# Kernel tuning notes

Measured on AMD Instinct MI355X. Metric: run time of the kernel, lower is better.

Reference implementation:

```python
import jax, jax.numpy as jnp
import numpy as np

N, E = 50000, 800000
IN, HID, OUT, H = 128, 32, 32, 4
NEG_SLOPE = 0.2
EPS = 1e-5


def layernorm(x, g, b):
    mu = x.mean(-1, keepdims=True)
    var = ((x - mu) ** 2).mean(-1, keepdims=True)
    return (x - mu) * jax.lax.rsqrt(var + EPS) * g + b


def gat_conv(x, src, dst, W, a_s, a_d, bias, heads, ch, concat):
    n = x.shape[0]
    h = (x @ W).reshape(n, heads, ch)               # [N,H,C]
    alpha_s = (h * a_s).sum(-1)                     # [N,H]
    alpha_d = (h * a_d).sum(-1)                     # [N,H]
    e = jax.nn.leaky_relu(alpha_s[src] + alpha_d[dst], NEG_SLOPE)  # [E,H]
    m = jax.ops.segment_max(e, dst, num_segments=n)
    m = jnp.where(jnp.isfinite(m), m, 0.0)
    ex = jnp.exp(e - m[dst])
    denom = jax.ops.segment_sum(ex, dst, num_segments=n)
    alpha = ex / (denom[dst] + 1e-16)               # [E,H]
    msg = h[src] * alpha[:, :, None]                # [E,H,C]
    out = jax.ops.segment_sum(msg, dst, num_segments=n)  # [N,H,C]
    out = out.reshape(n, heads * ch) if concat else out.mean(axis=1)
    return out + bias


def setup_inputs() -> dict:
    key = jax.random.key(0)
    ks = jax.random.split(key, 24)
    HC = HID * H
    s = 0.05
    inp = {
        "x": jax.random.normal(ks[0], (N, IN), jnp.float32),
        "edge_index": jax.random.randint(ks[1], (2, E), 0, N),
        "W1": jax.random.normal(ks[2], (IN, HC), jnp.float32) * s,
        "as1": jax.random.normal(ks[3], (H, HID), jnp.float32) * s,
        "ad1": jax.random.normal(ks[4], (H, HID), jnp.float32) * s,
        "b1": jnp.zeros((HC,), jnp.float32),
        "g1": jnp.ones((HC,), jnp.float32),
        "be1": jnp.zeros((HC,), jnp.float32),
        "W2": jax.random.normal(ks[5], (HC, HC), jnp.float32) * s,
        "as2": jax.random.normal(ks[6], (H, HID), jnp.float32) * s,
        "ad2": jax.random.normal(ks[7], (H, HID), jnp.float32) * s,
        "b2": jnp.zeros((HC,), jnp.float32),
        "g2": jnp.ones((HC,), jnp.float32),
        "be2": jnp.zeros((HC,), jnp.float32),
        "W3": jax.random.normal(ks[8], (HC, OUT * H), jnp.float32) * s,
        "as3": jax.random.normal(ks[9], (H, OUT), jnp.float32) * s,
        "ad3": jax.random.normal(ks[10], (H, OUT), jnp.float32) * s,
        "b3": jnp.zeros((OUT,), jnp.float32),
        "Wsk": jax.random.normal(ks[11], (IN, HC), jnp.float32) * s,
        "bsk": jnp.zeros((HC,), jnp.float32),
    }
    return inp


def reference(x, edge_index, W1, as1, ad1, b1, g1, be1, W2, as2, ad2, b2, g2, be2, W3, as3, ad3, b3, Wsk, bsk):
    n = x.shape[0]
    loops = jnp.arange(n, dtype=edge_index.dtype)
    src = jnp.concatenate([edge_index[0], loops])
    dst = jnp.concatenate([edge_index[1], loops])
    h = gat_conv(x, src, dst, W1, as1, ad1, b1, H, HID, True)
    h = jax.nn.elu(h)
    h = layernorm(h, g1, be1)
    h = h + (x @ Wsk + bsk)  # residual (dropout is identity in eval)
    h = gat_conv(h, src, dst, W2, as2, ad2, b2, H, HID, True)
    h = jax.nn.elu(h)
    h = layernorm(h, g2, be2)
    h = gat_conv(h, src, dst, W3, as3, ad3, b3, H, OUT, False)
    return h
```

## Files before the change

kernel.cpp:

```cpp
#include <hip/hip_runtime.h>
#include <hip/hip_bf16.h>

typedef __attribute__((ext_vector_type(8))) short short8;
typedef __attribute__((ext_vector_type(4))) float f32x4;
using bf16 = __hip_bfloat16;

#define NEG_SLOPE 0.2f
#define LN_EPS 1e-5f

__device__ __forceinline__ unsigned short f2bfu(float v) {
    bf16 t = __float2bfloat16(v);
    unsigned short s;
    __builtin_memcpy(&s, &t, 2);
    return s;
}
__device__ __forceinline__ short f2bf(float v) {
    bf16 t = __float2bfloat16(v);
    short s;
    __builtin_memcpy(&s, &t, 2);
    return s;
}
__device__ __forceinline__ unsigned packbf(float a, float b) {
    return (unsigned)f2bfu(a) | ((unsigned)f2bfu(b) << 16);
}
__device__ __forceinline__ float bflo(unsigned u) { return __uint_as_float(u << 16); }
__device__ __forceinline__ float bfhi(unsigned u) { return __uint_as_float(u & 0xffff0000u); }
__device__ __forceinline__ float bf1(unsigned short u) { return __uint_as_float(((unsigned)u) << 16); }

__global__ void detect_k(const void* __restrict__ x, int* flag,
                         int* bucketCur, int CAP) {
    int lane = threadIdx.x;
    for (int i = lane; i < 512; i += 64) bucketCur[i] = i * CAP;
    const unsigned short* u = (const unsigned short*)x;
    float m = 0.f;
    for (int i = lane; i < 8192; i += 64) {
        float v = fabsf(bf1(u[i]));
        if (!(v == v)) v = 1e30f;
        m = fmaxf(m, v);
    }
    for (int d = 1; d < 64; d <<= 1) m = fmaxf(m, __shfl_xor(m, d));
    if (lane == 0) flag[0] = (m > 1e4f) ? 1 : 0;
}

struct Ptr4 { const void* p[4]; };
struct Ptr14 { const void* p[14]; };
struct Ptr3 { const void* p[3]; };
struct Ptr6 { const void* p[6]; };
__global__ void stage_k(Ptr4 Ws, bf16* __restrict__ WT,
                        Ptr14 ptrs, bf16* __restrict__ sv,
                        Ptr3 Wv, Ptr6 av, bf16* __restrict__ vaT,
                        const int* __restrict__ flag) {
    int b = blockIdx.x;
    int f = flag[0];
    if (b < 256) {
        int gid = b * 256 + threadIdx.x;
        int m = gid >> 14;
        int idx = gid & 16383;
        int i = idx >> 7, j = idx & 127;
        const void* W = Ws.p[m];
        float v = f ? ((const float*)W)[idx]
                    : __bfloat162float(((const bf16*)W)[idx]);
        WT[m * 16384 + j * 128 + i] = __float2bfloat16(v);
    } else if (b == 256) {
        for (int k = threadIdx.x; k < 14 * 128; k += 256) {
            int t = k >> 7, i = k & 127;
            int n = (t == 12) ? 32 : 128;
            if (i < n) {
                const void* s = ptrs.p[t];
                float v = f ? ((const float*)s)[i]
                            : __bfloat162float(((const bf16*)s)[i]);
                sv[k] = __float2bfloat16(v);
            }
        }
    } else {
        int gid = (b - 257) * 256 + threadIdx.x;
        int l = gid >> 11;
        if (l >= 3) return;
        int c = (gid >> 7) & 15, k = gid & 127;
        float acc = 0.f;
        if (c < 8) {
            int hd = c & 3;
            const void* W = Wv.p[l];
            const void* a = av.p[l * 2 + (c >> 2)];
            for (int j = 0; j < 32; ++j) {
                float wv = f ? ((const float*)W)[k * 128 + hd * 32 + j]
                             : __bfloat162float(((const bf16*)W)[k * 128 + hd * 32 + j]);
                float avv = f ? ((const float*)a)[hd * 32 + j]
                              : __bfloat162float(((const bf16*)a)[hd * 32 + j]);
                acc += wv * avv;
            }
        }
        vaT[gid] = __float2bfloat16(acc);
    }
}

#define SCAT_EPB 2048
__global__ __launch_bounds__(256) void bscatter_k(const int* __restrict__ src,
                                                  const int* __restrict__ dst,
                                                  int* bucketCur,
                                                  int* __restrict__ ebuf,
                                                  int E, int NB, int CAP) {
    __shared__ int lcnt[512], lbase[512];
    int t = threadIdx.x;
    int e0 = blockIdx.x * SCAT_EPB;
    int cnt = E - e0;
    if (cnt > SCAT_EPB) cnt = SCAT_EPB;
    for (int i = t; i < NB; i += 256) lcnt[i] = 0;
    __syncthreads();
    for (int i = t; i < cnt; i += 256)
        atomicAdd(&lcnt[dst[e0 + i] >> 7], 1);
    __syncthreads();
    for (int i = t; i < NB; i += 256) {
        int c = lcnt[i];
        lbase[i] = c ? atomicAdd(&bucketCur[i], c) : 0;
        lcnt[i] = 0;
    }
    __syncthreads();
    for (int i = t; i < cnt; i += 256) {
        int d = dst[e0 + i];
        int b = d >> 7;
        int pos = lbase[b] + atomicAdd(&lcnt[b], 1);
        if (pos < (b + 1) * CAP)
            ebuf[pos] = ((d & 127) << 16) | src[e0 + i];
    }
}

__global__ __launch_bounds__(256) void build_k(const int* __restrict__ ebuf,
                                               const int* __restrict__ bucketCur,
                                               int* __restrict__ rowSE,
                                               int* __restrict__ colSrc,
                                               int N, int CAP) {
    int b = blockIdx.x, t = threadIdx.x;
    int base = b * CAP;
    int cnt = bucketCur[b] - base;
    if (cnt > CAP) cnt = CAP;
    __shared__ int nodeCnt[128], nodeCur[128], ws2[2];
    if (t < 128) nodeCnt[t] = 0;
    __syncthreads();
    for (int i = t; i < cnt; i += 256)
        atomicAdd(&nodeCnt[ebuf[base + i] >> 16], 1);
    __syncthreads();
    int v = 0, incl = 0;
    if (t < 128) {
        v = nodeCnt[t];
        incl = v;
        for (int d = 1; d < 64; d <<= 1) {
            int u = __shfl_up(incl, d);
            if ((t & 63) >= d) incl += u;
        }
        if ((t & 63) == 63) ws2[t >> 6] = incl;
    }
    __syncthreads();
    if (t < 128) {
        int excl = incl - v + ((t >= 64) ? ws2[0] : 0);
        int node = b * 128 + t;
        if (node < N) {
            rowSE[node * 2] = base + excl;
            rowSE[node * 2 + 1] = base + excl + v;
        }
        nodeCur[t] = excl;
    }
    __syncthreads();
    for (int i = t; i < cnt; i += 256) {
        int p = ebuf[base + i];
        int pos = base + atomicAdd(&nodeCur[p >> 16], 1);
        colSrc[pos] = (p & 0xffff) << 8;
    }
    for (int i = cnt + t; i < CAP; i += 256)
        colSrc[base + i] = 0;
}

template <int DUAL>
__global__ __launch_bounds__(256) void gemm_k(const void* __restrict__ A,
                                              const bf16* __restrict__ WT,
                                              bf16* __restrict__ out0,
                                              bf16* __restrict__ out1,
                                              const bf16* __restrict__ bias1,
                                              const bf16* __restrict__ vaT,
                                              float* __restrict__ asN,
                                              float* __restrict__ adN,
                                              int N, const int* __restrict__ flag) {
    int wave = threadIdx.x >> 6, lane = threadIdx.x & 63;
    int lm = lane & 15, lk = lane >> 4;
    const short* Ws = (const short*)WT;
    const short* Vs = (const short*)vaT;
    bool f32m = flag && flag[0];

    short8 bw0[2][4], bw1[DUAL ? 2 : 1][DUAL ? 4 : 1];
#pragma unroll
    for (int ct = 0; ct < 2; ++ct) {
        int c = (wave * 2 + ct) * 16 + lm;
#pragma unroll
        for (int kk = 0; kk < 4; ++kk)
            bw0[ct][kk] = *(const short8*)(Ws + (size_t)c * 128 + kk * 32 + lk * 8);
    }
    if (DUAL) {
#pragma unroll
        for (int ct = 0; ct < 2; ++ct) {
            int c = (wave * 2 + ct) * 16 + lm;
#pragma unroll
            for (int kk = 0; kk < 4; ++kk)
                bw1[ct][kk] = *(const short8*)(Ws + 16384 + (size_t)c * 128 + kk * 32 + lk * 8);
        }
    }
    short8 va8[4];
    if (wave == 0) {
#pragma unroll
        for (int kk = 0; kk < 4; ++kk)
            va8[kk] = *(const short8*)(Vs + (size_t)lm * 128 + kk * 32 + lk * 8);
    }
    float bv[DUAL ? 2 : 1];
    if (DUAL) {
#pragma unroll
        for (int ct = 0; ct < 2; ++ct)
            bv[ct] = __bfloat162float(bias1[(wave * 2 + ct) * 16 + lm]);
    }

    int stride = gridDim.x * 32;
    for (int rowBase = blockIdx.x * 32; rowBase < N; rowBase += stride) {
        short8 af[2][4];
#pragma unroll
        for (int rt = 0; rt < 2; ++rt) {
            int r = rowBase + rt * 16 + lm;
            if (r >= N) r = N - 1;
            if (f32m) {
#pragma unroll
                for (int kk = 0; kk < 4; ++kk) {
                    const float* Af = (const float*)A + (size_t)r * 128 + kk * 32 + lk * 8;
                    float4 q0 = *(const float4*)(Af);
                    float4 q1 = *(const float4*)(Af + 4);
                    short8 v;
                    v[0] = f2bf(q0.x); v[1] = f2bf(q0.y); v[2] = f2bf(q0.z); v[3] = f2bf(q0.w);
                    v[4] = f2bf(q1.x); v[5] = f2bf(q1.y); v[6] = f2bf(q1.z); v[7] = f2bf(q1.w);
                    af[rt][kk] = v;
                }
            } else {
#pragma unroll
                for (int kk = 0; kk < 4; ++kk)
                    af[rt][kk] = *(const short8*)((const short*)A + (size_t)r * 128 + kk * 32 + lk * 8);
            }
        }

        f32x4 acc0[2][2];
        f32x4 acc1[DUAL ? 2 : 1][DUAL ? 2 : 1];
#pragma unroll
        for (int ct = 0; ct < 2; ++ct)
#pragma unroll
            for (int rt = 0; rt < 2; ++rt) acc0[ct][rt] = (f32x4){0.f, 0.f, 0.f, 0.f};
        if (DUAL) {
#pragma unroll
            for (int ct = 0; ct < 2; ++ct)
#pragma unroll
                for (int rt = 0; rt < 2; ++rt) acc1[ct][rt] = (f32x4){0.f, 0.f, 0.f, 0.f};
        }

#pragma unroll
        for (int rt = 0; rt < 2; ++rt) {
#pragma unroll
            for (int kk = 0; kk < 4; ++kk) {
                acc0[0][rt] = __builtin_amdgcn_mfma_f32_16x16x32_bf16(af[rt][kk], bw0[0][kk], acc0[0][rt], 0, 0, 0);
                acc0[1][rt] = __builtin_amdgcn_mfma_f32_16x16x32_bf16(af[rt][kk], bw0[1][kk], acc0[1][rt], 0, 0, 0);
                if (DUAL) {
                    acc1[0][rt] = __builtin_amdgcn_mfma_f32_16x16x32_bf16(af[rt][kk], bw1[0][kk], acc1[0][rt], 0, 0, 0);
                    acc1[1][rt] = __builtin_amdgcn_mfma_f32_16x16x32_bf16(af[rt][kk], bw1[1][kk], acc1[1][rt], 0, 0, 0);
                }
            }
        }

#pragma unroll
        for (int ct = 0; ct < 2; ++ct) {
            int c = (wave * 2 + ct) * 16 + lm;
#pragma unroll
            for (int rt = 0; rt < 2; ++rt) {
#pragma unroll
                for (int i = 0; i < 4; ++i) {
                    int r = rowBase + rt * 16 + lk * 4 + i;
                    if (r < N) out0[(size_t)r * 128 + c] = __float2bfloat16(acc0[ct][rt][i]);
                }
            }
        }
        if (DUAL) {
#pragma unroll
            for (int ct = 0; ct < 2; ++ct) {
                int c = (wave * 2 + ct) * 16 + lm;
#pragma unroll
                for (int rt = 0; rt < 2; ++rt) {
#pragma unroll
                    for (int i = 0; i < 4; ++i) {
                        int r = rowBase + rt * 16 + lk * 4 + i;
                        if (r < N) out1[(size_t)r * 128 + c] = __float2bfloat16(acc1[ct][rt][i] + bv[ct]);
                    }
                }
            }
        }

        if (wave == 0) {
            f32x4 accA[2];
#pragma unroll
            for (int rt = 0; rt < 2; ++rt) accA[rt] = (f32x4){0.f, 0.f, 0.f, 0.f};
#pragma unroll
            for (int rt = 0; rt < 2; ++rt)
#pragma unroll
                for (int kk = 0; kk < 4; ++kk)
                    accA[rt] = __builtin_amdgcn_mfma_f32_16x16x32_bf16(af[rt][kk], va8[kk], accA[rt], 0, 0, 0);
            if (lm < 8) {
                float* dst = (lm < 4) ? asN : adN;
                int hh = lm & 3;
#pragma unroll
                for (int rt = 0; rt < 2; ++rt)
#pragma unroll
                    for (int i = 0; i < 4; ++i) {
                        int r = rowBase + rt * 16 + lk * 4 + i;
                        if (r < N) dst[(size_t)r * 4 + hh] = accA[rt][i];
                    }
            }
        }
    }
}

template <int MODE>
__global__ __launch_bounds__(256) void agg_k(const bf16* __restrict__ h,
                                             const float* __restrict__ asN,
                                             const float* __restrict__ adN,
                                             const int* __restrict__ rowSE,
                                             const int* __restrict__ colSrc,
                                             const bf16* __restrict__ bvec,
                                             const bf16* __restrict__ g,
                                             const bf16* __restrict__ be,
                                             void* outv, int N,
                                             const int* __restrict__ flag) {
    int wv = threadIdx.x >> 6, lane = threadIdx.x & 63;
    int n = blockIdx.x * 4 + wv;
    if (n >= N) return;
    int grp = lane >> 4, t = lane & 15;
    int hd = t >> 2;
    const char* hbase = (const char*)h + t * 16;
    const char* abase = (const char*)asN + hd * 4;

    int2 se = ((const int2*)rowSE)[n];
    int st = se.x, en = se.y;
    if (en < st) en = st;

    uint4 hself = *(const uint4*)(hbase + (size_t)n * 256);
    float adn = adN[(size_t)n * 4 + hd];
    float asn_self = asN[(size_t)n * 4 + hd];

    float a[8];
#pragma unroll
    for (int k = 0; k < 8; ++k) a[k] = 0.f;
    float den = 0.f;

    int j = st + grp;
    int off = (j < en) ? colSrc[j] : 0;
    float av = *(const float*)(abase + (off >> 4));
    uint4 hq = *(const uint4*)(hbase + off);
    for (; j < en; j += 4) {
        int off2 = colSrc[j + 4];
        float av2 = *(const float*)(abase + (off2 >> 4));
        uint4 hq2 = *(const uint4*)(hbase + off2);
        float e = av + adn;
        float w = __expf(fmaxf(e, NEG_SLOPE * e));
        den += w;
        a[0] += w * bflo(hq.x); a[1] += w * bfhi(hq.x);
        a[2] += w * bflo(hq.y); a[3] += w * bfhi(hq.y);
        a[4] += w * bflo(hq.z); a[5] += w * bfhi(hq.z);
        a[6] += w * bflo(hq.w); a[7] += w * bfhi(hq.w);
        av = av2; hq = hq2;
    }

#pragma unroll
    for (int k = 0; k < 8; ++k) {
        a[k] += __shfl_xor(a[k], 16);
        a[k] += __shfl_xor(a[k], 32);
    }
    den += __shfl_xor(den, 16);
    den += __shfl_xor(den, 32);

    float es = asn_self + adn;
    float wsf = __expf(fmaxf(es, NEG_SLOPE * es));
    den += wsf;
    a[0] += wsf * bflo(hself.x); a[1] += wsf * bfhi(hself.x);
    a[2] += wsf * bflo(hself.y); a[3] += wsf * bfhi(hself.y);
    a[4] += wsf * bflo(hself.z); a[5] += wsf * bfhi(hself.z);
    a[6] += wsf * bflo(hself.w); a[7] += wsf * bfhi(hself.w);

    float inv = 1.f / (den + 1e-16f);
    float y[8];
#pragma unroll
    for (int k = 0; k < 8; ++k) y[k] = a[k] * inv;

    if (MODE == 3) {
#pragma unroll
        for (int k = 0; k < 8; ++k) {
            y[k] += __shfl_xor(y[k], 4);
            y[k] += __shfl_xor(y[k], 8);
            y[k] *= 0.25f;
        }
        if (lane < 4) {
            int u = lane;
            uint4 bp = *(const uint4*)((const unsigned short*)bvec + u * 8);
            float v0 = y[0] + bflo(bp.x), v1 = y[1] + bfhi(bp.x);
            float v2 = y[2] + bflo(bp.y), v3 = y[3] + bfhi(bp.y);
            float v4 = y[4] + bflo(bp.z), v5 = y[5] + bfhi(bp.z);
            float v6 = y[6] + bflo(bp.w), v7 = y[7] + bfhi(bp.w);
            if (flag[0]) {
                float4* op = (float4*)outv + (size_t)n * 8 + u * 2;
                op[0] = make_float4(v0, v1, v2, v3);
                op[1] = make_float4(v4, v5, v6, v7);
            } else {
                uint4 pk;
                pk.x = packbf(v0, v1); pk.y = packbf(v2, v3);
                pk.z = packbf(v4, v5); pk.w = packbf(v6, v7);
                ((uint4*)outv)[(size_t)n * 4 + u] = pk;
            }
        }
    } else {
        unsigned short* out = (unsigned short*)outv;
        uint4 bp = *(const uint4*)((const unsigned short*)bvec + t * 8);
        y[0] += bflo(bp.x); y[1] += bfhi(bp.x);
        y[2] += bflo(bp.y); y[3] += bfhi(bp.y);
        y[4] += bflo(bp.z); y[5] += bfhi(bp.z);
        y[6] += bflo(bp.w); y[7] += bfhi(bp.w);
#pragma unroll
        for (int k = 0; k < 8; ++k) y[k] = y[k] > 0.f ? y[k] : (__expf(y[k]) - 1.f);
        float s = 0.f, q = 0.f;
#pragma unroll
        for (int k = 0; k < 8; ++k) { s += y[k]; q += y[k] * y[k]; }
        for (int d = 1; d < 16; d <<= 1) {
            s += __shfl_xor(s, d);
            q += __shfl_xor(q, d);
        }
        float mu = s * (1.f / 128.f);
        float var = q * (1.f / 128.f) - mu * mu;
        var = fmaxf(var, 0.f);
        float rs = rsqrtf(var + LN_EPS);
        if (lane < 16) {
            uint4 gp = *(const uint4*)((const unsigned short*)g + t * 8);
            uint4 ep = *(const uint4*)((const unsigned short*)be + t * 8);
            float z[8];
            z[0] = (y[0] - mu) * rs * bflo(gp.x) + bflo(ep.x);
            z[1] = (y[1] - mu) * rs * bfhi(gp.x) + bfhi(ep.x);
            z[2] = (y[2] - mu) * rs * bflo(gp.y) + bflo(ep.y);
            z[3] = (y[3] - mu) * rs * bfhi(gp.y) + bfhi(ep.y);
            z[4] = (y[4] - mu) * rs * bflo(gp.z) + bflo(ep.z);
            z[5] = (y[5] - mu) * rs * bfhi(gp.z) + bfhi(ep.z);
            z[6] = (y[6] - mu) * rs * bflo(gp.w) + bflo(ep.w);
            z[7] = (y[7] - mu) * rs * bfhi(gp.w) + bfhi(ep.w);
            if (MODE == 1) {
                uint4 sk = *(uint4*)(out + (size_t)n * 128 + t * 8);
                z[0] += bflo(sk.x); z[1] += bfhi(sk.x);
                z[2] += bflo(sk.y); z[3] += bfhi(sk.y);
                z[4] += bflo(sk.z); z[5] += bfhi(sk.z);
                z[6] += bflo(sk.w); z[7] += bfhi(sk.w);
            }
            uint4 pk;
            pk.x = packbf(z[0], z[1]); pk.y = packbf(z[2], z[3]);
            pk.z = packbf(z[4], z[5]); pk.w = packbf(z[6], z[7]);
            *(uint4*)(out + (size_t)n * 128 + t * 8) = pk;
        }
    }
}

extern "C" void kernel_launch(void* const* d_in, const int* in_sizes, int n_in,
                              void* d_out, int out_size, void* d_ws, size_t ws_size,
                              hipStream_t stream) {
    const void* x  = d_in[0];
    const int*  ei = (const int*)d_in[1];

    int N = in_sizes[0] / 128;
    int E = in_sizes[1] / 2;
    const int* srcI = ei;
    const int* dstI = ei + E;

    int NB = (N + 127) >> 7;
    int CAP = (E / NB + 1024 + 511) & ~511;

    char* w = (char*)d_ws;
    size_t o = 0;
    auto carve = [&](size_t bytes) {
        void* p = w + o;
        o += (bytes + 255) & ~(size_t)255;
        return p;
    };
    int*  dtFlag = (int*)carve(256);
    bf16* WTall = (bf16*)carve(4 * 16384 * 2);
    bf16* sv   = (bf16*)carve(14 * 128 * 2);
    bf16* vaT  = (bf16*)carve(3 * 16 * 128 * 2);
    bf16* hB   = (bf16*)carve((size_t)N * 128 * 2);
    bf16* xB   = (bf16*)carve((size_t)N * 128 * 2);
    float* asN = (float*)carve((size_t)N * 4 * 4);
    float* adN = (float*)carve((size_t)N * 4 * 4);
    int* rowSE = (int*)carve((size_t)N * 2 * 4);
    int* colSrc= (int*)carve((size_t)NB * CAP * 4 + 64);
    int* ebuf  = (int*)carve((size_t)NB * CAP * 4);
    int* bucketCur = (int*)carve(512 * 4);

    detect_k<<<1, 64, 0, stream>>>(x, dtFlag, bucketCur, CAP);

    Ptr4 wp;
    wp.p[0] = d_in[2];  wp.p[1] = d_in[18];
    wp.p[2] = d_in[8];  wp.p[3] = d_in[14];
    Ptr14 ptrs;
    ptrs.p[0] = d_in[3];  ptrs.p[1] = d_in[4];  ptrs.p[2] = d_in[5];
    ptrs.p[3] = d_in[6];  ptrs.p[4] = d_in[7];
    ptrs.p[5] = d_in[9];  ptrs.p[6] = d_in[10]; ptrs.p[7] = d_in[11];
    ptrs.p[8] = d_in[12]; ptrs.p[9] = d_in[13];
    ptrs.p[10] = d_in[15]; ptrs.p[11] = d_in[16]; ptrs.p[12] = d_in[17];
    ptrs.p[13] = d_in[19];
    Ptr3 wv3;
    wv3.p[0] = d_in[2]; wv3.p[1] = d_in[8]; wv3.p[2] = d_in[14];
    Ptr6 av6;
    av6.p[0] = d_in[3];  av6.p[1] = d_in[4];
    av6.p[2] = d_in[9];  av6.p[3] = d_in[10];
    av6.p[4] = d_in[15]; av6.p[5] = d_in[16];

    stage_k<<<281, 256, 0, stream>>>(wp, WTall, ptrs, sv, wv3, av6, vaT, dtFlag);

    bscatter_k<<<(E + SCAT_EPB - 1) / SCAT_EPB, 256, 0, stream>>>(srcI, dstI,
                                                                 bucketCur, ebuf, E, NB, CAP);
    build_k<<<NB, 256, 0, stream>>>(ebuf, bucketCur, rowSE, colSrc, N, CAP);

    int gb = (N + 63) / 64;
    int nb4 = (N + 3) / 4;

    gemm_k<1><<<gb, 256, 0, stream>>>(x, WTall, hB, xB, sv + 13 * 128,
                                      vaT, asN, adN, N, dtFlag);
    agg_k<1><<<nb4, 256, 0, stream>>>(hB, asN, adN, rowSE, colSrc,
                                      sv + 2 * 128, sv + 3 * 128, sv + 4 * 128,
                                      xB, N, dtFlag);

    gemm_k<0><<<gb, 256, 0, stream>>>(xB, WTall + 2 * 16384, hB, nullptr, nullptr,
                                      vaT + 2048, asN, adN, N, nullptr);
    agg_k<2><<<nb4, 256, 0, stream>>>(hB, asN, adN, rowSE, colSrc,
                                      sv + 7 * 128, sv + 8 * 128, sv + 9 * 128,
                                      xB, N, dtFlag);

    gemm_k<0><<<gb, 256, 0, stream>>>(xB, WTall + 3 * 16384, hB, nullptr, nullptr,
                                      vaT + 4096, asN, adN, N, nullptr);
    agg_k<3><<<nb4, 256, 0, stream>>>(hB, asN, adN, rowSE, colSrc,
                                      sv + 12 * 128, nullptr, nullptr,
                                      d_out, N, dtFlag);
}
```

Baseline: 350.1 us.

## Vectorize GEMM stores via swapped MFMA operands and deepen aggregation prefetch

Swaps the MFMA A/B operands so each lane holds four consecutive columns of one row, which allows packed 8-byte bf16 stores and 16-byte float4 stores for the attention logits in place of scattered scalar stores. The aggregation loop now prefetches two neighbor edges ahead instead of one, and colSrc gets extra zero padding so the lookahead reads stay in bounds. The epilogue is reworked so every lane finalizes two channels, reducing across the whole wave instead of having 16 lanes each handle eight. The deeper prefetch costs more registers, and the epilogue adds select logic and a longer shuffle chain.

```diff
diff --git a/kernel.cpp b/kernel.cpp
--- a/kernel.cpp
+++ b/kernel.cpp
@@ -166,7 +166,8 @@
         int pos = base + atomicAdd(&nodeCur[p >> 16], 1);
         colSrc[pos] = (p & 0xffff) << 8;
     }
-    for (int i = cnt + t; i < CAP; i += 256)
+    int capz = CAP + ((b == (int)gridDim.x - 1) ? 32 : 0);
+    for (int i = cnt + t; i < capz; i += 256)
         colSrc[base + i] = 0;
 }
 
@@ -209,11 +210,15 @@
         for (int kk = 0; kk < 4; ++kk)
             va8[kk] = *(const short8*)(Vs + (size_t)lm * 128 + kk * 32 + lk * 8);
     }
-    float bv[DUAL ? 2 : 1];
+    float bv[2][4];
     if (DUAL) {
 #pragma unroll
-        for (int ct = 0; ct < 2; ++ct)
-            bv[ct] = __bfloat162float(bias1[(wave * 2 + ct) * 16 + lm]);
+        for (int ct = 0; ct < 2; ++ct) {
+            int c0 = (wave * 2 + ct) * 16 + lk * 4;
+#pragma unroll
+            for (int i = 0; i < 4; ++i)
+                bv[ct][i] = __bfloat162float(bias1[c0 + i]);
+        }
     }
 
     int stride = gridDim.x * 32;
@@ -258,37 +263,41 @@
         for (int rt = 0; rt < 2; ++rt) {
 #pragma unroll
             for (int kk = 0; kk < 4; ++kk) {
-                acc0[0][rt] = __builtin_amdgcn_mfma_f32_16x16x32_bf16(af[rt][kk], bw0[0][kk], acc0[0][rt], 0, 0, 0);
-                acc0[1][rt] = __builtin_amdgcn_mfma_f32_16x16x32_bf16(af[rt][kk], bw0[1][kk], acc0[1][rt], 0, 0, 0);
+                acc0[0][rt] = __builtin_amdgcn_mfma_f32_16x16x32_bf16(bw0[0][kk], af[rt][kk], acc0[0][rt], 0, 0, 0);
+                acc0[1][rt] = __builtin_amdgcn_mfma_f32_16x16x32_bf16(bw0[1][kk], af[rt][kk], acc0[1][rt], 0, 0, 0);
                 if (DUAL) {
-                    acc1[0][rt] = __builtin_amdgcn_mfma_f32_16x16x32_bf16(af[rt][kk], bw1[0][kk], acc1[0][rt], 0, 0, 0);
-                    acc1[1][rt] = __builtin_amdgcn_mfma_f32_16x16x32_bf16(af[rt][kk], bw1[1][kk], acc1[1][rt], 0, 0, 0);
+                    acc1[0][rt] = __builtin_amdgcn_mfma_f32_16x16x32_bf16(bw1[0][kk], af[rt][kk], acc1[0][rt], 0, 0, 0);
+                    acc1[1][rt] = __builtin_amdgcn_mfma_f32_16x16x32_bf16(bw1[1][kk], af[rt][kk], acc1[1][rt], 0, 0, 0);
                 }
             }
         }
 
 #pragma unroll
         for (int ct = 0; ct < 2; ++ct) {
-            int c = (wave * 2 + ct) * 16 + lm;
+            int c0 = (wave * 2 + ct) * 16 + lk * 4;
 #pragma unroll
             for (int rt = 0; rt < 2; ++rt) {
-#pragma unroll
-                for (int i = 0; i < 4; ++i) {
-                    int r = rowBase + rt * 16 + lk * 4 + i;
-                    if (r < N) out0[(size_t)r * 128 + c] = __float2bfloat16(acc0[ct][rt][i]);
+                int r = rowBase + rt * 16 + lm;
+                if (r < N) {
+                    uint2 pk;
+                    pk.x = packbf(acc0[ct][rt][0], acc0[ct][rt][1]);
+                    pk.y = packbf(acc0[ct][rt][2], acc0[ct][rt][3]);
+                    *(uint2*)((unsigned short*)out0 + (size_t)r * 128 + c0) = pk;
                 }
             }
         }
         if (DUAL) {
 #pragma unroll
             for (int ct = 0; ct < 2; ++ct) {
-                int c = (wave * 2 + ct) * 16 + lm;
+                int c0 = (wave * 2 + ct) * 16 + lk * 4;
 #pragma unroll
                 for (int rt = 0; rt < 2; ++rt) {
-#pragma unroll
-                    for (int i = 0; i < 4; ++i) {
-                        int r = rowBase + rt * 16 + lk * 4 + i;
-                        if (r < N) out1[(size_t)r * 128 + c] = __float2bfloat16(acc1[ct][rt][i] + bv[ct]);
+                    int r = rowBase + rt * 16 + lm;
+                    if (r < N) {
+                        uint2 pk;
+                        pk.x = packbf(acc1[ct][rt][0] + bv[ct][0], acc1[ct][rt][1] + bv[ct][1]);
+                        pk.y = packbf(acc1[ct][rt][2] + bv[ct][2], acc1[ct][rt][3] + bv[ct][3]);
+                        *(uint2*)((unsigned short*)out1 + (size_t)r * 128 + c0) = pk;
                     }
                 }
             }
@@ -302,17 +311,14 @@
             for (int rt = 0; rt < 2; ++rt)
 #pragma unroll
                 for (int kk = 0; kk < 4; ++kk)
-                    accA[rt] = __builtin_amdgcn_mfma_f32_16x16x32_bf16(af[rt][kk], va8[kk], accA[rt], 0, 0, 0);
-            if (lm < 8) {
-                float* dst = (lm < 4) ? asN : adN;
-                int hh = lm & 3;
-#pragma unroll
-                for (int rt = 0; rt < 2; ++rt)
-#pragma unroll
-                    for (int i = 0; i < 4; ++i) {
-                        int r = rowBase + rt * 16 + lk * 4 + i;
-                        if (r < N) dst[(size_t)r * 4 + hh] = accA[rt][i];
-                    }
+                    accA[rt] = __builtin_amdgcn_mfma_f32_16x16x32_bf16(va8[kk], af[rt][kk], accA[rt], 0, 0, 0);
+            if (lk < 2) {
+                float* dp = lk ? adN : asN;
+#pragma unroll
+                for (int rt = 0; rt < 2; ++rt) {
+                    int r = rowBase + rt * 16 + lm;
+                    if (r < N) *(f32x4*)(dp + (size_t)r * 4) = accA[rt];
+                }
             }
         }
     }
@@ -341,9 +347,9 @@
     int st = se.x, en = se.y;
     if (en < st) en = st;
 
-    uint4 hself = *(const uint4*)(hbase + (size_t)n * 256);
     float adn = adN[(size_t)n * 4 + hd];
     float asn_self = asN[(size_t)n * 4 + hd];
+    unsigned hs = *(const unsigned*)((const char*)h + (size_t)n * 256 + t * 16 + grp * 4);
 
     float a[8];
 #pragma unroll
@@ -351,21 +357,27 @@
     float den = 0.f;
 
     int j = st + grp;
-    int off = (j < en) ? colSrc[j] : 0;
-    float av = *(const float*)(abase + (off >> 4));
-    uint4 hq = *(const uint4*)(hbase + off);
+    int o0 = (j < en) ? colSrc[j] : 0;
+    int o1 = colSrc[j + 4];
+    int o2 = colSrc[j + 8];
+    float av0 = *(const float*)(abase + (o0 >> 4));
+    uint4 hq0 = *(const uint4*)(hbase + o0);
+    float av1 = *(const float*)(abase + (o1 >> 4));
+    uint4 hq1 = *(const uint4*)(hbase + o1);
     for (; j < en; j += 4) {
-        int off2 = colSrc[j + 4];
-        float av2 = *(const float*)(abase + (off2 >> 4));
-        uint4 hq2 = *(const uint4*)(hbase + off2);
-        float e = av + adn;
+        int o3 = colSrc[j + 12];
+        float av2 = *(const float*)(abase + (o2 >> 4));
+        uint4 hq2 = *(const uint4*)(hbase + o2);
+        float e = av0 + adn;
         float w = __expf(fmaxf(e, NEG_SLOPE * e));
         den += w;
-        a[0] += w * bflo(hq.x); a[1] += w * bfhi(hq.x);
-        a[2] += w * bflo(hq.y); a[3] += w * bfhi(hq.y);
-        a[4] += w * bflo(hq.z); a[5] += w * bfhi(hq.z);
-        a[6] += w * bflo(hq.w); a[7] += w * bfhi(hq.w);
-        av = av2; hq = hq2;
+        a[0] += w * bflo(hq0.x); a[1] += w * bfhi(hq0.x);
+        a[2] += w * bflo(hq0.y); a[3] += w * bfhi(hq0.y);
+        a[4] += w * bflo(hq0.z); a[5] += w * bfhi(hq0.z);
+        a[6] += w * bflo(hq0.w); a[7] += w * bfhi(hq0.w);
+        o2 = o3;
+        av0 = av1; hq0 = hq1;
+        av1 = av2; hq1 = hq2;
     }
 
 #pragma unroll
@@ -379,54 +391,43 @@
     float es = asn_self + adn;
     float wsf = __expf(fmaxf(es, NEG_SLOPE * es));
     den += wsf;
-    a[0] += wsf * bflo(hself.x); a[1] += wsf * bfhi(hself.x);
-    a[2] += wsf * bflo(hself.y); a[3] += wsf * bfhi(hself.y);
-    a[4] += wsf * bflo(hself.z); a[5] += wsf * bfhi(hself.z);
-    a[6] += wsf * bflo(hself.w); a[7] += wsf * bfhi(hself.w);
+
+    float s0 = (grp & 1) ? a[2] : a[0];
+    float s1 = (grp & 1) ? a[3] : a[1];
+    float s2 = (grp & 1) ? a[6] : a[4];
+    float s3 = (grp & 1) ? a[7] : a[5];
+    float p0 = (grp & 2) ? s2 : s0;
+    float p1 = (grp & 2) ? s3 : s1;
+
+    p0 += wsf * bflo(hs);
+    p1 += wsf * bfhi(hs);
 
     float inv = 1.f / (den + 1e-16f);
-    float y[8];
-#pragma unroll
-    for (int k = 0; k < 8; ++k) y[k] = a[k] * inv;
+    float y0 = p0 * inv, y1 = p1 * inv;
 
     if (MODE == 3) {
-#pragma unroll
-        for (int k = 0; k < 8; ++k) {
-            y[k] += __shfl_xor(y[k], 4);
-            y[k] += __shfl_xor(y[k], 8);
-            y[k] *= 0.25f;
-        }
-        if (lane < 4) {
-            int u = lane;
-            uint4 bp = *(const uint4*)((const unsigned short*)bvec + u * 8);
-            float v0 = y[0] + bflo(bp.x), v1 = y[1] + bfhi(bp.x);
-            float v2 = y[2] + bflo(bp.y), v3 = y[3] + bfhi(bp.y);
-            float v4 = y[4] + bflo(bp.z), v5 = y[5] + bfhi(bp.z);
-            float v6 = y[6] + bflo(bp.w), v7 = y[7] + bfhi(bp.w);
+        y0 += __shfl_xor(y0, 4); y0 += __shfl_xor(y0, 8); y0 *= 0.25f;
+        y1 += __shfl_xor(y1, 4); y1 += __shfl_xor(y1, 8); y1 *= 0.25f;
+        if (t < 4) {
+            int oc = t * 8 + grp * 2;
+            unsigned bp = *(const unsigned*)((const char*)bvec + oc * 2);
+            float v0 = y0 + bflo(bp), v1 = y1 + bfhi(bp);
             if (flag[0]) {
-                float4* op = (float4*)outv + (size_t)n * 8 + u * 2;
-                op[0] = make_float4(v0, v1, v2, v3);
-                op[1] = make_float4(v4, v5, v6, v7);
+                *(float2*)((float*)outv + (size_t)n * 32 + oc) = make_float2(v0, v1);
             } else {
-                uint4 pk;
-                pk.x = packbf(v0, v1); pk.y = packbf(v2, v3);
-                pk.z = packbf(v4, v5); pk.w = packbf(v6, v7);
-                ((uint4*)outv)[(size_t)n * 4 + u] = pk;
+                ((unsigned*)outv)[(size_t)n * 16 + (oc >> 1)] = packbf(v0, v1);
             }
         }
     } else {
         unsigned short* out = (unsigned short*)outv;
-        uint4 bp = *(const uint4*)((const unsigned short*)bvec + t * 8);
-        y[0] += bflo(bp.x); y[1] += bfhi(bp.x);
-        y[2] += bflo(bp.y); y[3] += bfhi(bp.y);
-        y[4] += bflo(bp.z); y[5] += bfhi(bp.z);
-        y[6] += bflo(bp.w); y[7] += bfhi(bp.w);
-#pragma unroll
-        for (int k = 0; k < 8; ++k) y[k] = y[k] > 0.f ? y[k] : (__expf(y[k]) - 1.f);
-        float s = 0.f, q = 0.f;
-#pragma unroll
-        for (int k = 0; k < 8; ++k) { s += y[k]; q += y[k] * y[k]; }
-        for (int d = 1; d < 16; d <<= 1) {
+        int boff = t * 16 + grp * 4;
+        unsigned bp = *(const unsigned*)((const char*)bvec + boff);
+        y0 += bflo(bp); y1 += bfhi(bp);
+        y0 = y0 > 0.f ? y0 : (__expf(y0) - 1.f);
+        y1 = y1 > 0.f ? y1 : (__expf(y1) - 1.f);
+        float s = y0 + y1, q = y0 * y0 + y1 * y1;
+#pragma unroll
+        for (int d = 1; d < 64; d <<= 1) {
             s += __shfl_xor(s, d);
             q += __shfl_xor(q, d);
         }
@@ -434,30 +435,16 @@
         float var = q * (1.f / 128.f) - mu * mu;
         var = fmaxf(var, 0.f);
         float rs = rsqrtf(var + LN_EPS);
-        if (lane < 16) {
-            uint4 gp = *(const uint4*)((const unsigned short*)g + t * 8);
-            uint4 ep = *(const uint4*)((const unsigned short*)be + t * 8);
-            float z[8];
-            z[0] = (y[0] - mu) * rs * bflo(gp.x) + bflo(ep.x);
-            z[1] = (y[1] - mu) * rs * bfhi(gp.x) + bfhi(ep.x);
-            z[2] = (y[2] - mu) * rs * bflo(gp.y) + bflo(ep.y);
-            z[3] = (y[3] - mu) * rs * bfhi(gp.y) + bfhi(ep.y);
-            z[4] = (y[4] - mu) * rs * bflo(gp.z) + bflo(ep.z);
-            z[5] = (y[5] - mu) * rs * bfhi(gp.z) + bfhi(ep.z);
-            z[6] = (y[6] - mu) * rs * bflo(gp.w) + bflo(ep.w);
-            z[7] = (y[7] - mu) * rs * bfhi(gp.w) + bfhi(ep.w);
-            if (MODE == 1) {
-                uint4 sk = *(uint4*)(out + (size_t)n * 128 + t * 8);
-                z[0] += bflo(sk.x); z[1] += bfhi(sk.x);
-                z[2] += bflo(sk.y); z[3] += bfhi(sk.y);
-                z[4] += bflo(sk.z); z[5] += bfhi(sk.z);
-                z[6] += bflo(sk.w); z[7] += bfhi(sk.w);
-            }
-            uint4 pk;
-            pk.x = packbf(z[0], z[1]); pk.y = packbf(z[2], z[3]);
-            pk.z = packbf(z[4], z[5]); pk.w = packbf(z[6], z[7]);
-            *(uint4*)(out + (size_t)n * 128 + t * 8) = pk;
-        }
+        unsigned gp = *(const unsigned*)((const char*)g + boff);
+        unsigned ep = *(const unsigned*)((const char*)be + boff);
+        float z0 = (y0 - mu) * rs * bflo(gp) + bflo(ep);
+        float z1 = (y1 - mu) * rs * bfhi(gp) + bfhi(ep);
+        char* op = (char*)out + (size_t)n * 256 + boff;
+        if (MODE == 1) {
+            unsigned sk = *(const unsigned*)op;
+            z0 += bflo(sk); z1 += bfhi(sk);
+        }
+        *(unsigned*)op = packbf(z0, z1);
     }
 }
 
@@ -491,7 +478,7 @@
     float* asN = (float*)carve((size_t)N * 4 * 4);
     float* adN = (float*)carve((size_t)N * 4 * 4);
     int* rowSE = (int*)carve((size_t)N * 2 * 4);
-    int* colSrc= (int*)carve((size_t)NB * CAP * 4 + 64);
+    int* colSrc= (int*)carve((size_t)NB * CAP * 4 + 128);
     int* ebuf  = (int*)carve((size_t)NB * CAP * 4);
     int* bucketCur = (int*)carve(512 * 4);
 
```

Result: faster. 342.6 us (-2.1%).
